# Kernel tuning notes

Measured on AMD Instinct MI355X. Metric: run time of the kernel, lower is better.

The kernel has to match this reference:

```python
import jax, jax.numpy as jnp
import numpy as np

DIM = 768
HEADS = 12
HIDDEN = int(DIM * 4.0)


def layernorm(x, w, b, eps=1e-5):
    mu = jnp.mean(x, axis=-1, keepdims=True)
    var = jnp.var(x, axis=-1, keepdims=True)
    return (x - mu) * jax.lax.rsqrt(var + eps) * w + b


def setup_inputs() -> dict:
    key = jax.random.key(0)
    ks = jax.random.split(key, 16)
    B, Nq, Nc, D = 4, 1024, 1024, DIM
    s = 0.02
    return {
        "query_tokens": jax.random.normal(ks[0], (B, Nq, D), jnp.float32),
        "context_tokens": jax.random.normal(ks[1], (B, Nc, D), jnp.float32),
        "wind_bias": jax.random.normal(ks[2], (B, 1, Nq, Nc), jnp.float32),
        "ln_q_w": jnp.ones((D,), jnp.float32), "ln_q_b": jnp.zeros((D,), jnp.float32),
        "ln_kv_w": jnp.ones((D,), jnp.float32), "ln_kv_b": jnp.zeros((D,), jnp.float32),
        "Wq": jax.random.normal(ks[3], (D, D), jnp.float32) * s, "bq": jnp.zeros((D,), jnp.float32),
        "Wk": jax.random.normal(ks[4], (D, D), jnp.float32) * s, "bk": jnp.zeros((D,), jnp.float32),
        "Wv": jax.random.normal(ks[5], (D, D), jnp.float32) * s, "bv": jnp.zeros((D,), jnp.float32),
        "Wo": jax.random.normal(ks[6], (D, D), jnp.float32) * s, "bo": jnp.zeros((D,), jnp.float32),
        "beta": jnp.ones((HEADS, 1, 1), jnp.float32),
        "ln_f_w": jnp.ones((D,), jnp.float32), "ln_f_b": jnp.zeros((D,), jnp.float32),
        "W1": jax.random.normal(ks[7], (D, HIDDEN), jnp.float32) * s, "b1": jnp.zeros((HIDDEN,), jnp.float32),
        "W2": jax.random.normal(ks[8], (HIDDEN, D), jnp.float32) * s, "b2": jnp.zeros((D,), jnp.float32),
    }


def reference(query_tokens, context_tokens, wind_bias,
              ln_q_w, ln_q_b, ln_kv_w, ln_kv_b,
              Wq, bq, Wk, bk, Wv, bv, Wo, bo, beta,
              ln_f_w, ln_f_b, W1, b1, W2, b2):
    B, Nq, D = query_tokens.shape
    H = HEADS
    hd = D // H
    scale = hd ** -0.5

    q = layernorm(query_tokens, ln_q_w, ln_q_b) @ Wq + bq
    kv = layernorm(context_tokens, ln_kv_w, ln_kv_b)
    k = kv @ Wk + bk
    v = kv @ Wv + bv

    # [B, H, N, hd]
    q = q.reshape(B, Nq, H, hd).transpose(0, 2, 1, 3)
    k = k.reshape(B, -1, H, hd).transpose(0, 2, 1, 3)
    v = v.reshape(B, -1, H, hd).transpose(0, 2, 1, 3)

    attn = jnp.einsum('bhqd,bhkd->bhqk', q * scale, k)
    attn = attn + beta * wind_bias  # beta: [H,1,1] broadcasts over [B,H,Nq,Nc]
    attn = jax.nn.softmax(attn.astype(jnp.float32), axis=-1).astype(q.dtype)

    out = jnp.einsum('bhqk,bhkd->bhqd', attn, v).transpose(0, 2, 1, 3).reshape(B, Nq, D)
    out = out @ Wo + bo

    x = query_tokens + out
    h = layernorm(x, ln_f_w, ln_f_b)
    h = jax.nn.gelu(h @ W1 + b1, approximate=False) @ W2 + b2
    return x + h
```

## Files before the change

### kernel.cpp

```cpp
#include <hip/hip_runtime.h>
#include <hip/hip_bf16.h>


#define DIM 768
#define HID 3072
#define NHEAD 12
#define BATCH 4
#define SEQ 1024
#define ROWS (BATCH * SEQ)
#define HD 64

typedef __attribute__((ext_vector_type(8))) __bf16 bf16x8;
typedef __attribute__((ext_vector_type(4))) float f32x4;
typedef __attribute__((ext_vector_type(4))) unsigned int u32x4;

#define MFMA16(a, b, c) __builtin_amdgcn_mfma_f32_16x16x32_bf16((a), (b), (c), 0, 0, 0)

#define GLDS16(g, l)                                                         \
  __builtin_amdgcn_global_load_lds(                                          \
      (const __attribute__((address_space(1))) void*)(g),                    \
      (__attribute__((address_space(3))) void*)(l), 16, 0, 0)

__device__ __forceinline__ unsigned pk2(float lo, float hi) {
  unsigned a = __bfloat16_as_ushort(__float2bfloat16(lo));
  unsigned b = __bfloat16_as_ushort(__float2bfloat16(hi));
  return a | (b << 16);
}

__global__ __launch_bounds__(256) void wg_transpose(const float* __restrict__ W,
                                                    __hip_bfloat16* __restrict__ WT,
                                                    int K, int N) {
  __shared__ float tile[32][33];
  const int tx = threadIdx.x & 31, ty = threadIdx.x >> 5;
  const int n0 = blockIdx.x * 32, k0 = blockIdx.y * 32;
#pragma unroll
  for (int i = 0; i < 4; i++)
    tile[ty + i * 8][tx] = W[(size_t)(k0 + ty + i * 8) * N + n0 + tx];
  __syncthreads();
#pragma unroll
  for (int i = 0; i < 4; i++)
    WT[(size_t)(n0 + ty + i * 8) * K + k0 + tx] = __float2bfloat16(tile[tx][ty + i * 8]);
}

__global__ void wg_bcat(const float* __restrict__ bq, const float* __restrict__ bk,
                        const float* __restrict__ bv, float* __restrict__ bc) {
  int i = blockIdx.x * 256 + threadIdx.x;
  if (i < 768) bc[i] = bq[i];
  else if (i < 1536) bc[i] = bk[i - 768];
  else if (i < 2304) bc[i] = bv[i - 1536];
}

__global__ __launch_bounds__(256) void wg_ln(const float* __restrict__ in,
                                             const float* __restrict__ w,
                                             const float* __restrict__ b,
                                             __hip_bfloat16* __restrict__ out) {
  int row = blockIdx.x;
  int t = threadIdx.x;
  const float* p = in + (size_t)row * DIM;
  float v0 = p[t], v1 = p[t + 256], v2 = p[t + 512];
  float s = v0 + v1 + v2;
  float q = v0 * v0 + v1 * v1 + v2 * v2;
#pragma unroll
  for (int d = 1; d < 64; d <<= 1) {
    s += __shfl_xor(s, d);
    q += __shfl_xor(q, d);
  }
  __shared__ float ss[4], sq[4];
  if ((t & 63) == 0) {
    ss[t >> 6] = s;
    sq[t >> 6] = q;
  }
  __syncthreads();
  s = ss[0] + ss[1] + ss[2] + ss[3];
  q = sq[0] + sq[1] + sq[2] + sq[3];
  float mu = s * (1.0f / DIM);
  float var = q * (1.0f / DIM) - mu * mu;
  float rs = rsqrtf(var + 1e-5f);
  __hip_bfloat16* o = out + (size_t)row * DIM;
  o[t] = __float2bfloat16((v0 - mu) * rs * w[t] + b[t]);
  o[t + 256] = __float2bfloat16((v1 - mu) * rs * w[t + 256] + b[t + 256]);
  o[t + 512] = __float2bfloat16((v2 - mu) * rs * w[t + 512] + b[t + 512]);
}

template <int MODE>
__global__ __launch_bounds__(512) void wg_gemm(const __hip_bfloat16* __restrict__ A,
                                               const __hip_bfloat16* __restrict__ BT,
                                               const float* __restrict__ bias,
                                               void* __restrict__ Cout,
                                               const float* __restrict__ resid,
                                               float* __restrict__ aux,
                                               int N, int Kloop, int Kstride, float p0) {
  __shared__ __hip_bfloat16 As[128 * 64];
  __shared__ __hip_bfloat16 Bs[128 * 64];
  const int t = threadIdx.x;
  const int lane = t & 63;
  const int wave = t >> 6;
  const int wr = wave >> 1, wc = wave & 1;
  const int lhi = lane >> 4, llo = lane & 15;
  const int nbn = N >> 7;
  const int bm = blockIdx.x / nbn, bn = blockIdx.x % nbn;
  const int koff = (MODE == 7) ? blockIdx.y * Kloop : 0;

  const __hip_bfloat16* Ause = A;
  if (MODE == 6 && bn >= 6) Ause = A + (size_t)ROWS * DIM;

  const int s0 = t, s1 = t + 512;
  const int sr0 = s0 >> 3, sg0 = ((s0 & 7) ^ (sr0 & 7)) * 8;
  const int sr1 = s1 >> 3, sg1 = ((s1 & 7) ^ (sr1 & 7)) * 8;
  const __hip_bfloat16* Ag = Ause + (size_t)(bm * 128) * Kstride + koff;
  const __hip_bfloat16* Bg = BT + (size_t)(bn * 128) * Kstride + koff;

  f32x4 zero = {0.f, 0.f, 0.f, 0.f};
  f32x4 acc[2][4];
#pragma unroll
  for (int i = 0; i < 2; i++)
#pragma unroll
    for (int j = 0; j < 4; j++) acc[i][j] = zero;

  for (int k0 = 0; k0 < Kloop; k0 += 64) {
    __syncthreads();
    GLDS16(Ag + (size_t)sr0 * Kstride + k0 + sg0, As + s0 * 8);
    GLDS16(Ag + (size_t)sr1 * Kstride + k0 + sg1, As + s1 * 8);
    GLDS16(Bg + (size_t)sr0 * Kstride + k0 + sg0, Bs + s0 * 8);
    GLDS16(Bg + (size_t)sr1 * Kstride + k0 + sg1, Bs + s1 * 8);
    __syncthreads();
    bf16x8 af[2][2], bfr[4][2];
#pragma unroll
    for (int i = 0; i < 2; i++) {
      const int row = wr * 32 + i * 16 + llo;
#pragma unroll
      for (int kk = 0; kk < 2; kk++)
        af[i][kk] = *reinterpret_cast<const bf16x8*>(
            &As[row * 64 + (((kk * 4 + lhi) ^ (row & 7)) << 3)]);
    }
#pragma unroll
    for (int j = 0; j < 4; j++) {
      const int row = wc * 64 + j * 16 + llo;
#pragma unroll
      for (int kk = 0; kk < 2; kk++)
        bfr[j][kk] = *reinterpret_cast<const bf16x8*>(
            &Bs[row * 64 + (((kk * 4 + lhi) ^ (row & 7)) << 3)]);
    }
    __builtin_amdgcn_s_setprio(1);
#pragma unroll
    for (int kk = 0; kk < 2; kk++)
#pragma unroll
      for (int i = 0; i < 2; i++)
#pragma unroll
        for (int j = 0; j < 4; j++)
          acc[i][j] = MFMA16(af[i][kk], bfr[j][kk], acc[i][j]);
    __builtin_amdgcn_s_setprio(0);
  }

#pragma unroll
  for (int i = 0; i < 2; i++) {
    int gr = bm * 128 + wr * 32 + i * 16 + lhi * 4;
#pragma unroll
    for (int j = 0; j < 4; j++) {
      int gc = bn * 128 + wc * 64 + j * 16 + llo;
      float bv_ = (MODE == 7) ? 0.f : bias[gc];
#pragma unroll
      for (int r = 0; r < 4; r++) {
        float v = acc[i][j][r] + bv_;
        int row = gr + r;
        size_t idx = (size_t)row * N + gc;
        if (MODE == 3) {
          aux[idx] = resid[idx] + v;
        } else if (MODE == 4) {
          ((__hip_bfloat16*)Cout)[idx] =
              __float2bfloat16(v * 0.5f * (1.0f + erff(v * 0.70710678118f)));
        } else if (MODE == 7) {
          aux[(size_t)blockIdx.y * ROWS * N + idx] = v;
        } else if (MODE == 6) {
          int sec = gc / 768;
          int n2 = gc - sec * 768;
          __hip_bfloat16* base = (__hip_bfloat16*)Cout;
          if (sec == 0) {
            base[(size_t)row * DIM + n2] = __float2bfloat16(v * p0);
          } else if (sec == 1) {
            base[(size_t)ROWS * DIM + (size_t)row * DIM + n2] = __float2bfloat16(v);
          } else {
            int b_ = row >> 10, n_ = row & 1023;
            int h_ = n2 >> 6, d_ = n2 & 63;
            base[(size_t)2 * ROWS * DIM +
                 (((size_t)(b_ * NHEAD + h_) * HD + d_) << 10) + n_] = __float2bfloat16(v);
          }
        }
      }
    }
  }
}

template <int NP>
__global__ __launch_bounds__(256) void wg_red(const float* __restrict__ partial,
                                              const float* __restrict__ resid,
                                              const float* __restrict__ bias,
                                              float* __restrict__ out) {
  const int i = blockIdx.x * 256 + threadIdx.x;
  const int NF4 = ROWS * DIM / 4;
  if (i >= NF4) return;
  const f32x4* P = (const f32x4*)partial;
  f32x4 p = P[i];
#pragma unroll
  for (int c = 1; c < NP; c++) p += P[i + c * NF4];
  f32x4 r = ((const f32x4*)resid)[i];
  f32x4 bv = ((const f32x4*)bias)[i % (DIM / 4)];
  ((f32x4*)out)[i] = r + p + bv;
}

__global__ __launch_bounds__(256) void wg_attn4(const __hip_bfloat16* __restrict__ Q,
                                                const __hip_bfloat16* __restrict__ Kb,
                                                const __hip_bfloat16* __restrict__ Vt,
                                                const float* __restrict__ wb,
                                                const float* __restrict__ beta,
                                                __hip_bfloat16* __restrict__ O) {
  __shared__ __hip_bfloat16 Ks[2][4096];
  __shared__ __hip_bfloat16 Vs[2][4096];
  const int t = threadIdx.x;
  const int lane = t & 63;
  const int lhi = lane >> 4, llo = lane & 15;

  const int bid = blockIdx.x;
  const int wid = (bid & 7) * 96 + (bid >> 3);
  const int h = wid % NHEAD;
  const int g = wid / NHEAD;
  const int qt = g & 15;
  const int b = g >> 4;
  const float betah = beta[h] * 1.44269504089f;

  const int w = t >> 6;
  const size_t qrow0 = (size_t)b * SEQ + qt * 64 + w * 16;
  const __hip_bfloat16* Qp = Q + qrow0 * DIM + h * HD;
  bf16x8 a0 = *reinterpret_cast<const bf16x8*>(&Qp[(size_t)llo * DIM + lhi * 8]);
  bf16x8 a1 = *reinterpret_cast<const bf16x8*>(&Qp[(size_t)llo * DIM + 32 + lhi * 8]);

  const __hip_bfloat16* Kg = Kb + (size_t)b * SEQ * DIM + h * HD;
  const __hip_bfloat16* Vg = Vt + (size_t)(b * NHEAD + h) * HD * SEQ;
  const float* wrow = wb + (qrow0 + llo) * SEQ;

  const int slot0 = t, slot1 = t + 256;
  const int r0 = slot0 >> 3, c0 = (slot0 & 7) ^ (r0 & 7);
  const int r1 = slot1 >> 3, c1 = (slot1 & 7) ^ (r1 & 7);

  auto stage = [&](int buf, int kb) {
    GLDS16(Kg + (size_t)(kb + r0) * DIM + c0 * 8, &Ks[buf][slot0 * 8]);
    GLDS16(Kg + (size_t)(kb + r1) * DIM + c1 * 8, &Ks[buf][slot1 * 8]);
    GLDS16(Vg + (size_t)r0 * SEQ + kb + c0 * 8, &Vs[buf][slot0 * 8]);
    GLDS16(Vg + (size_t)r1 * SEQ + kb + c1 * 8, &Vs[buf][slot1 * 8]);
  };

  f32x4 zero = {0.f, 0.f, 0.f, 0.f};
  f32x4 oc[4];
#pragma unroll
  for (int c = 0; c < 4; c++) oc[c] = zero;
  float m_ = -1e30f, l_ = 0.f;

  f32x4 wv[4];
#pragma unroll
  for (int c2 = 0; c2 < 4; c2++)
    wv[c2] = *reinterpret_cast<const f32x4*>(&wrow[c2 * 16 + lhi * 4]);

  stage(0, 0);
  __syncthreads();
  int cur = 0;

  const int srcA = (lane & 15) | ((lane & 16) << 1);
  const bool chi = (lane & 32) != 0;

  for (int kt = 0; kt < SEQ / 64; kt++) {
    const int kb = kt * 64;
    f32x4 wvn[4];
    if (kt < SEQ / 64 - 1) {
      stage(cur ^ 1, kb + 64);
#pragma unroll
      for (int c2 = 0; c2 < 4; c2++)
        wvn[c2] = *reinterpret_cast<const f32x4*>(&wrow[kb + 64 + c2 * 16 + lhi * 4]);
    }

    f32x4 sv[4];
    __builtin_amdgcn_s_setprio(1);
#pragma unroll
    for (int c2 = 0; c2 < 4; c2++) {
      const int row = c2 * 16 + llo;
      bf16x8 k0 = *reinterpret_cast<const bf16x8*>(
          &Ks[cur][((row << 3) + (lhi ^ (row & 7))) << 3]);
      bf16x8 k1 = *reinterpret_cast<const bf16x8*>(
          &Ks[cur][((row << 3) + ((4 + lhi) ^ (row & 7))) << 3]);
      f32x4 s_ = zero;
      s_ = MFMA16(k0, a0, s_);
      s_ = MFMA16(k1, a1, s_);
      sv[c2] = s_;
    }
    __builtin_amdgcn_s_setprio(0);

#pragma unroll
    for (int c2 = 0; c2 < 4; c2++)
#pragma unroll
      for (int r = 0; r < 4; r++) sv[c2][r] += betah * wv[c2][r];

    float mx;
    {
      f32x4 m4;
#pragma unroll
      for (int r = 0; r < 4; r++)
        m4[r] = fmaxf(fmaxf(sv[0][r], sv[1][r]), fmaxf(sv[2][r], sv[3][r]));
      mx = fmaxf(fmaxf(m4[0], m4[1]), fmaxf(m4[2], m4[3]));
      mx = fmaxf(mx, __shfl_xor(mx, 16));
      mx = fmaxf(mx, __shfl_xor(mx, 32));
    }

    const bool grow = __any(mx > m_);
    float corr = 1.f;
    if (grow) {
      float mn = fmaxf(m_, mx);
      corr = exp2f(m_ - mn);
      m_ = mn;
    }

#pragma unroll
    for (int c2 = 0; c2 < 4; c2++)
#pragma unroll
      for (int r = 0; r < 4; r++) sv[c2][r] = exp2f(sv[c2][r] - m_);
    f32x4 s4;
#pragma unroll
    for (int r = 0; r < 4; r++) s4[r] = (sv[0][r] + sv[1][r]) + (sv[2][r] + sv[3][r]);
    float rs = (s4[0] + s4[1]) + (s4[2] + s4[3]);
    rs += __shfl_xor(rs, 16);
    rs += __shfl_xor(rs, 32);
    l_ = l_ * corr + rs;

    if (grow) {
      float cr[4];
#pragma unroll
      for (int r = 0; r < 4; r++) cr[r] = __shfl(corr, lhi * 4 + r);
#pragma unroll
      for (int c = 0; c < 4; c++)
#pragma unroll
        for (int r = 0; r < 4; r++) oc[c][r] *= cr[r];
    }

    unsigned p01[4], p23[4];
#pragma unroll
    for (int c2 = 0; c2 < 4; c2++) {
      p01[c2] = pk2(sv[c2][0], sv[c2][1]);
      p23[c2] = pk2(sv[c2][2], sv[c2][3]);
    }
    unsigned a01_0A = (unsigned)__shfl((int)p01[0], srcA);
    unsigned a01_1A = (unsigned)__shfl((int)p01[1], srcA);
    unsigned a23_0A = (unsigned)__shfl((int)p23[0], srcA);
    unsigned a23_1A = (unsigned)__shfl((int)p23[1], srcA);
    unsigned a01_0B = (unsigned)__shfl((int)p01[0], srcA + 16);
    unsigned a01_1B = (unsigned)__shfl((int)p01[1], srcA + 16);
    unsigned a23_0B = (unsigned)__shfl((int)p23[0], srcA + 16);
    unsigned a23_1B = (unsigned)__shfl((int)p23[1], srcA + 16);
    unsigned b01_2A = (unsigned)__shfl((int)p01[2], srcA);
    unsigned b01_3A = (unsigned)__shfl((int)p01[3], srcA);
    unsigned b23_2A = (unsigned)__shfl((int)p23[2], srcA);
    unsigned b23_3A = (unsigned)__shfl((int)p23[3], srcA);
    unsigned b01_2B = (unsigned)__shfl((int)p01[2], srcA + 16);
    unsigned b01_3B = (unsigned)__shfl((int)p01[3], srcA + 16);
    unsigned b23_2B = (unsigned)__shfl((int)p23[2], srcA + 16);
    unsigned b23_3B = (unsigned)__shfl((int)p23[3], srcA + 16);
    u32x4 t0, t1;
    t0[0] = chi ? a01_1A : a01_0A;
    t0[1] = chi ? a23_1A : a23_0A;
    t0[2] = chi ? a01_1B : a01_0B;
    t0[3] = chi ? a23_1B : a23_0B;
    t1[0] = chi ? b01_3A : b01_2A;
    t1[1] = chi ? b23_3A : b23_2A;
    t1[2] = chi ? b01_3B : b01_2B;
    t1[3] = chi ? b23_3B : b23_2B;
    bf16x8 pf0 = __builtin_bit_cast(bf16x8, t0);
    bf16x8 pf1 = __builtin_bit_cast(bf16x8, t1);

    __builtin_amdgcn_s_setprio(1);
#pragma unroll
    for (int c = 0; c < 4; c++) {
      const int row = c * 16 + llo;
      bf16x8 v0 = *reinterpret_cast<const bf16x8*>(
          &Vs[cur][((row << 3) + (lhi ^ (row & 7))) << 3]);
      bf16x8 v1 = *reinterpret_cast<const bf16x8*>(
          &Vs[cur][((row << 3) + ((4 + lhi) ^ (row & 7))) << 3]);
      oc[c] = MFMA16(pf0, v0, oc[c]);
      oc[c] = MFMA16(pf1, v1, oc[c]);
    }
    __builtin_amdgcn_s_setprio(0);

    if (kt < SEQ / 64 - 1) {
#pragma unroll
      for (int c2 = 0; c2 < 4; c2++) wv[c2] = wvn[c2];
    }
    __syncthreads();
    cur ^= 1;
  }

  float iv[4];
  float invl = 1.0f / l_;
#pragma unroll
  for (int r = 0; r < 4; r++) iv[r] = __shfl(invl, lhi * 4 + r);
  __hip_bfloat16* Op = O + qrow0 * DIM + h * HD;
#pragma unroll
  for (int c = 0; c < 4; c++)
#pragma unroll
    for (int r = 0; r < 4; r++)
      Op[(size_t)(lhi * 4 + r) * DIM + c * 16 + llo] = __float2bfloat16(oc[c][r] * iv[r]);
}

extern "C" void kernel_launch(void* const* d_in, const int* in_sizes, int n_in,
                              void* d_out, int out_size, void* d_ws, size_t ws_size,
                              hipStream_t stream) {
  const float* query = (const float*)d_in[0];
  const float* context = (const float*)d_in[1];
  const float* wind = (const float*)d_in[2];
  const float* ln_q_w = (const float*)d_in[3];
  const float* ln_q_b = (const float*)d_in[4];
  const float* ln_kv_w = (const float*)d_in[5];
  const float* ln_kv_b = (const float*)d_in[6];
  const float* Wq = (const float*)d_in[7];
  const float* bq = (const float*)d_in[8];
  const float* Wk = (const float*)d_in[9];
  const float* bk = (const float*)d_in[10];
  const float* Wv = (const float*)d_in[11];
  const float* bv = (const float*)d_in[12];
  const float* Wo = (const float*)d_in[13];
  const float* bo = (const float*)d_in[14];
  const float* beta = (const float*)d_in[15];
  const float* ln_f_w = (const float*)d_in[16];
  const float* ln_f_b = (const float*)d_in[17];
  const float* W1 = (const float*)d_in[18];
  const float* b1 = (const float*)d_in[19];
  const float* W2 = (const float*)d_in[20];
  const float* b2 = (const float*)d_in[21];
  float* out = (float*)d_out;

  char* ws = (char*)d_ws;
  size_t off = 0;
  auto take = [&](size_t bytes) -> char* {
    char* p = ws + off;
    off += (bytes + 255) & ~(size_t)255;
    return p;
  };
  const size_t actB = (size_t)ROWS * DIM * 2;
  __hip_bfloat16* qln = (__hip_bfloat16*)take(actB);
  __hip_bfloat16* kvln = (__hip_bfloat16*)take(actB);
  __hip_bfloat16* qb = (__hip_bfloat16*)take(actB);
  __hip_bfloat16* kbuf = (__hip_bfloat16*)take(actB);
  __hip_bfloat16* vt = (__hip_bfloat16*)take(actB);
  __hip_bfloat16* aout = (__hip_bfloat16*)take(actB);
  __hip_bfloat16* hbuf = (__hip_bfloat16*)take(actB);
  float* xbuf = (float*)take((size_t)ROWS * DIM * 4);
  __hip_bfloat16* hid = (__hip_bfloat16*)take((size_t)ROWS * HID * 2);
  __hip_bfloat16* WqT = (__hip_bfloat16*)take((size_t)DIM * DIM * 2);
  __hip_bfloat16* WkT = (__hip_bfloat16*)take((size_t)DIM * DIM * 2);
  __hip_bfloat16* WvT = (__hip_bfloat16*)take((size_t)DIM * DIM * 2);
  __hip_bfloat16* WoT = (__hip_bfloat16*)take((size_t)DIM * DIM * 2);
  __hip_bfloat16* W1T = (__hip_bfloat16*)take((size_t)DIM * HID * 2);
  __hip_bfloat16* W2T = (__hip_bfloat16*)take((size_t)HID * DIM * 2);
  float* bcat = (float*)take(2304 * 4);
  float* kpart = (float*)take((size_t)4 * ROWS * DIM * 4);

  wg_transpose<<<dim3(24, 24), 256, 0, stream>>>(Wq, WqT, DIM, DIM);
  wg_transpose<<<dim3(24, 24), 256, 0, stream>>>(Wk, WkT, DIM, DIM);
  wg_transpose<<<dim3(24, 24), 256, 0, stream>>>(Wv, WvT, DIM, DIM);
  wg_transpose<<<dim3(24, 24), 256, 0, stream>>>(Wo, WoT, DIM, DIM);
  wg_transpose<<<dim3(96, 24), 256, 0, stream>>>(W1, W1T, DIM, HID);
  wg_transpose<<<dim3(24, 96), 256, 0, stream>>>(W2, W2T, HID, DIM);
  wg_bcat<<<9, 256, 0, stream>>>(bq, bk, bv, bcat);

  wg_ln<<<ROWS, 256, 0, stream>>>(query, ln_q_w, ln_q_b, qln);
  wg_ln<<<ROWS, 256, 0, stream>>>(context, ln_kv_w, ln_kv_b, kvln);

  const float scale = 0.125f * 1.44269504089f;
  wg_gemm<6><<<32 * 18, 512, 0, stream>>>(qln, WqT, bcat, qb, nullptr, nullptr,
                                          2304, DIM, DIM, scale);

  wg_attn4<<<768, 256, 0, stream>>>(qb, kbuf, vt, wind, beta, aout);

  const int g768 = (ROWS / 128) * (DIM / 128);
  const int g3072 = (ROWS / 128) * (HID / 128);
  wg_gemm<3><<<g768, 512, 0, stream>>>(aout, WoT, bo, nullptr, query, xbuf, DIM, DIM, DIM, 0.f);
  wg_ln<<<ROWS, 256, 0, stream>>>(xbuf, ln_f_w, ln_f_b, hbuf);
  wg_gemm<4><<<g3072, 512, 0, stream>>>(hbuf, W1T, b1, hid, nullptr, nullptr, HID, DIM, DIM, 0.f);
  wg_gemm<7><<<dim3(g768, 4), 512, 0, stream>>>(hid, W2T, nullptr, nullptr, nullptr, kpart,
                                                DIM, HID / 4, HID, 0.f);
  wg_red<4><<<(ROWS * DIM / 4 + 255) / 256, 256, 0, stream>>>(kpart, xbuf, b2, out);
}
```

Before: 225.2 us.

## Split attention KV tiles across waves with merged softmax and approximate GELU

The attention kernel now assigns each block 32 query rows and splits every 64-key tile between two wave pairs, halving per-wave score work and doubling the grid to raise parallelism. Partial outputs and softmax statistics are merged through shared memory at the end, and the P·V MFMA operand order is swapped so rescaling uses a per-lane scalar. The FFN GELU epilogue replaces erff with a sigmoid-of-cubic approximation to cut transcendental cost. This adds K/V reload traffic per query and introduces a small numeric deviation from exact GELU.

```diff
diff --git a/kernel.cpp b/kernel.cpp
--- a/kernel.cpp
+++ b/kernel.cpp
@@ -13,6 +13,7 @@
 typedef __attribute__((ext_vector_type(8))) __bf16 bf16x8;
 typedef __attribute__((ext_vector_type(4))) float f32x4;
 typedef __attribute__((ext_vector_type(4))) unsigned int u32x4;
+typedef __attribute__((ext_vector_type(2))) unsigned int u32x2;
 
 #define MFMA16(a, b, c) __builtin_amdgcn_mfma_f32_16x16x32_bf16((a), (b), (c), 0, 0, 0)
 
@@ -167,8 +168,10 @@
         if (MODE == 3) {
           aux[idx] = resid[idx] + v;
         } else if (MODE == 4) {
-          ((__hip_bfloat16*)Cout)[idx] =
-              __float2bfloat16(v * 0.5f * (1.0f + erff(v * 0.70710678118f)));
+          float x3 = v * v * v;
+          float z = -2.302208f * v - 0.102943f * x3;
+          float g = v / (1.0f + exp2f(z));
+          ((__hip_bfloat16*)Cout)[idx] = __float2bfloat16(g);
         } else if (MODE == 7) {
           aux[(size_t)blockIdx.y * ROWS * N + idx] = v;
         } else if (MODE == 6) {
@@ -208,7 +211,7 @@
   ((f32x4*)out)[i] = r + p + bv;
 }
 
-__global__ __launch_bounds__(256) void wg_attn4(const __hip_bfloat16* __restrict__ Q,
+__global__ __launch_bounds__(256) void wg_attn5(const __hip_bfloat16* __restrict__ Q,
                                                 const __hip_bfloat16* __restrict__ Kb,
                                                 const __hip_bfloat16* __restrict__ Vt,
                                                 const float* __restrict__ wb,
@@ -219,17 +222,19 @@
   const int t = threadIdx.x;
   const int lane = t & 63;
   const int lhi = lane >> 4, llo = lane & 15;
+  const int w = t >> 6;
+  const int wq = w & 1;
+  const int wk = w >> 1;
 
   const int bid = blockIdx.x;
-  const int wid = (bid & 7) * 96 + (bid >> 3);
+  const int wid = (bid & 7) * 192 + (bid >> 3);
   const int h = wid % NHEAD;
   const int g = wid / NHEAD;
-  const int qt = g & 15;
-  const int b = g >> 4;
+  const int qt = g & 31;
+  const int b = g >> 5;
   const float betah = beta[h] * 1.44269504089f;
 
-  const int w = t >> 6;
-  const size_t qrow0 = (size_t)b * SEQ + qt * 64 + w * 16;
+  const size_t qrow0 = (size_t)b * SEQ + qt * 32 + wq * 16;
   const __hip_bfloat16* Qp = Q + qrow0 * DIM + h * HD;
   bf16x8 a0 = *reinterpret_cast<const bf16x8*>(&Qp[(size_t)llo * DIM + lhi * 8]);
   bf16x8 a1 = *reinterpret_cast<const bf16x8*>(&Qp[(size_t)llo * DIM + 32 + lhi * 8]);
@@ -255,10 +260,12 @@
   for (int c = 0; c < 4; c++) oc[c] = zero;
   float m_ = -1e30f, l_ = 0.f;
 
-  f32x4 wv[4];
-#pragma unroll
-  for (int c2 = 0; c2 < 4; c2++)
-    wv[c2] = *reinterpret_cast<const f32x4*>(&wrow[c2 * 16 + lhi * 4]);
+  const int kvo = wk * 32;
+
+  f32x4 wv[2];
+#pragma unroll
+  for (int c2 = 0; c2 < 2; c2++)
+    wv[c2] = *reinterpret_cast<const f32x4*>(&wrow[kvo + c2 * 16 + lhi * 4]);
 
   stage(0, 0);
   __syncthreads();
@@ -269,19 +276,19 @@
 
   for (int kt = 0; kt < SEQ / 64; kt++) {
     const int kb = kt * 64;
-    f32x4 wvn[4];
+    f32x4 wvn[2];
     if (kt < SEQ / 64 - 1) {
       stage(cur ^ 1, kb + 64);
 #pragma unroll
-      for (int c2 = 0; c2 < 4; c2++)
-        wvn[c2] = *reinterpret_cast<const f32x4*>(&wrow[kb + 64 + c2 * 16 + lhi * 4]);
-    }
-
-    f32x4 sv[4];
+      for (int c2 = 0; c2 < 2; c2++)
+        wvn[c2] = *reinterpret_cast<const f32x4*>(&wrow[kb + 64 + kvo + c2 * 16 + lhi * 4]);
+    }
+
+    f32x4 sv[2];
     __builtin_amdgcn_s_setprio(1);
 #pragma unroll
-    for (int c2 = 0; c2 < 4; c2++) {
-      const int row = c2 * 16 + llo;
+    for (int c2 = 0; c2 < 2; c2++) {
+      const int row = kvo + c2 * 16 + llo;
       bf16x8 k0 = *reinterpret_cast<const bf16x8*>(
           &Ks[cur][((row << 3) + (lhi ^ (row & 7))) << 3]);
       bf16x8 k1 = *reinterpret_cast<const bf16x8*>(
@@ -294,7 +301,7 @@
     __builtin_amdgcn_s_setprio(0);
 
 #pragma unroll
-    for (int c2 = 0; c2 < 4; c2++)
+    for (int c2 = 0; c2 < 2; c2++)
 #pragma unroll
       for (int r = 0; r < 4; r++) sv[c2][r] += betah * wv[c2][r];
 
@@ -302,8 +309,7 @@
     {
       f32x4 m4;
 #pragma unroll
-      for (int r = 0; r < 4; r++)
-        m4[r] = fmaxf(fmaxf(sv[0][r], sv[1][r]), fmaxf(sv[2][r], sv[3][r]));
+      for (int r = 0; r < 4; r++) m4[r] = fmaxf(sv[0][r], sv[1][r]);
       mx = fmaxf(fmaxf(m4[0], m4[1]), fmaxf(m4[2], m4[3]));
       mx = fmaxf(mx, __shfl_xor(mx, 16));
       mx = fmaxf(mx, __shfl_xor(mx, 32));
@@ -318,92 +324,97 @@
     }
 
 #pragma unroll
-    for (int c2 = 0; c2 < 4; c2++)
+    for (int c2 = 0; c2 < 2; c2++)
 #pragma unroll
       for (int r = 0; r < 4; r++) sv[c2][r] = exp2f(sv[c2][r] - m_);
     f32x4 s4;
 #pragma unroll
-    for (int r = 0; r < 4; r++) s4[r] = (sv[0][r] + sv[1][r]) + (sv[2][r] + sv[3][r]);
+    for (int r = 0; r < 4; r++) s4[r] = sv[0][r] + sv[1][r];
     float rs = (s4[0] + s4[1]) + (s4[2] + s4[3]);
     rs += __shfl_xor(rs, 16);
     rs += __shfl_xor(rs, 32);
     l_ = l_ * corr + rs;
 
     if (grow) {
-      float cr[4];
-#pragma unroll
-      for (int r = 0; r < 4; r++) cr[r] = __shfl(corr, lhi * 4 + r);
 #pragma unroll
       for (int c = 0; c < 4; c++)
 #pragma unroll
-        for (int r = 0; r < 4; r++) oc[c][r] *= cr[r];
-    }
-
-    unsigned p01[4], p23[4];
-#pragma unroll
-    for (int c2 = 0; c2 < 4; c2++) {
+        for (int r = 0; r < 4; r++) oc[c][r] *= corr;
+    }
+
+    unsigned p01[2], p23[2];
+#pragma unroll
+    for (int c2 = 0; c2 < 2; c2++) {
       p01[c2] = pk2(sv[c2][0], sv[c2][1]);
       p23[c2] = pk2(sv[c2][2], sv[c2][3]);
     }
-    unsigned a01_0A = (unsigned)__shfl((int)p01[0], srcA);
-    unsigned a01_1A = (unsigned)__shfl((int)p01[1], srcA);
-    unsigned a23_0A = (unsigned)__shfl((int)p23[0], srcA);
-    unsigned a23_1A = (unsigned)__shfl((int)p23[1], srcA);
-    unsigned a01_0B = (unsigned)__shfl((int)p01[0], srcA + 16);
-    unsigned a01_1B = (unsigned)__shfl((int)p01[1], srcA + 16);
-    unsigned a23_0B = (unsigned)__shfl((int)p23[0], srcA + 16);
-    unsigned a23_1B = (unsigned)__shfl((int)p23[1], srcA + 16);
-    unsigned b01_2A = (unsigned)__shfl((int)p01[2], srcA);
-    unsigned b01_3A = (unsigned)__shfl((int)p01[3], srcA);
-    unsigned b23_2A = (unsigned)__shfl((int)p23[2], srcA);
-    unsigned b23_3A = (unsigned)__shfl((int)p23[3], srcA);
-    unsigned b01_2B = (unsigned)__shfl((int)p01[2], srcA + 16);
-    unsigned b01_3B = (unsigned)__shfl((int)p01[3], srcA + 16);
-    unsigned b23_2B = (unsigned)__shfl((int)p23[2], srcA + 16);
-    unsigned b23_3B = (unsigned)__shfl((int)p23[3], srcA + 16);
-    u32x4 t0, t1;
-    t0[0] = chi ? a01_1A : a01_0A;
-    t0[1] = chi ? a23_1A : a23_0A;
-    t0[2] = chi ? a01_1B : a01_0B;
-    t0[3] = chi ? a23_1B : a23_0B;
-    t1[0] = chi ? b01_3A : b01_2A;
-    t1[1] = chi ? b23_3A : b23_2A;
-    t1[2] = chi ? b01_3B : b01_2B;
-    t1[3] = chi ? b23_3B : b23_2B;
-    bf16x8 pf0 = __builtin_bit_cast(bf16x8, t0);
-    bf16x8 pf1 = __builtin_bit_cast(bf16x8, t1);
+    unsigned P01_0A = (unsigned)__shfl((int)p01[0], srcA);
+    unsigned P01_1A = (unsigned)__shfl((int)p01[1], srcA);
+    unsigned P23_0A = (unsigned)__shfl((int)p23[0], srcA);
+    unsigned P23_1A = (unsigned)__shfl((int)p23[1], srcA);
+    unsigned P01_0B = (unsigned)__shfl((int)p01[0], srcA + 16);
+    unsigned P01_1B = (unsigned)__shfl((int)p01[1], srcA + 16);
+    unsigned P23_0B = (unsigned)__shfl((int)p23[0], srcA + 16);
+    unsigned P23_1B = (unsigned)__shfl((int)p23[1], srcA + 16);
+    u32x4 tb;
+    tb[0] = chi ? P01_1A : P01_0A;
+    tb[1] = chi ? P23_1A : P23_0A;
+    tb[2] = chi ? P01_1B : P01_0B;
+    tb[3] = chi ? P23_1B : P23_0B;
+    bf16x8 pB = __builtin_bit_cast(bf16x8, tb);
 
     __builtin_amdgcn_s_setprio(1);
 #pragma unroll
     for (int c = 0; c < 4; c++) {
       const int row = c * 16 + llo;
-      bf16x8 v0 = *reinterpret_cast<const bf16x8*>(
-          &Vs[cur][((row << 3) + (lhi ^ (row & 7))) << 3]);
-      bf16x8 v1 = *reinterpret_cast<const bf16x8*>(
-          &Vs[cur][((row << 3) + ((4 + lhi) ^ (row & 7))) << 3]);
-      oc[c] = MFMA16(pf0, v0, oc[c]);
-      oc[c] = MFMA16(pf1, v1, oc[c]);
+      const int ch = (wk * 4 + lhi) ^ (row & 7);
+      bf16x8 vf = *reinterpret_cast<const bf16x8*>(&Vs[cur][((row << 3) + ch) << 3]);
+      oc[c] = MFMA16(vf, pB, oc[c]);
     }
     __builtin_amdgcn_s_setprio(0);
 
     if (kt < SEQ / 64 - 1) {
-#pragma unroll
-      for (int c2 = 0; c2 < 4; c2++) wv[c2] = wvn[c2];
+      wv[0] = wvn[0];
+      wv[1] = wvn[1];
     }
     __syncthreads();
     cur ^= 1;
   }
 
-  float iv[4];
-  float invl = 1.0f / l_;
-#pragma unroll
-  for (int r = 0; r < 4; r++) iv[r] = __shfl(invl, lhi * 4 + r);
-  __hip_bfloat16* Op = O + qrow0 * DIM + h * HD;
-#pragma unroll
-  for (int c = 0; c < 4; c++)
-#pragma unroll
-    for (int r = 0; r < 4; r++)
-      Op[(size_t)(lhi * 4 + r) * DIM + c * 16 + llo] = __float2bfloat16(oc[c][r] * iv[r]);
+  float* Obuf = (float*)&Ks[0][0];
+  float* Sbuf = (float*)&Vs[0][0];
+  if (wk == 1) {
+    if (lhi == 0) {
+      Sbuf[wq * 32 + llo] = m_;
+      Sbuf[wq * 32 + 16 + llo] = l_;
+    }
+    float* ob = Obuf + wq * 16 * 68 + llo * 68;
+#pragma unroll
+    for (int c = 0; c < 4; c++)
+      *reinterpret_cast<f32x4*>(&ob[c * 16 + lhi * 4]) = oc[c];
+  }
+  __syncthreads();
+  if (wk == 0) {
+    float m1 = Sbuf[wq * 32 + llo];
+    float l1 = Sbuf[wq * 32 + 16 + llo];
+    float mf = fmaxf(m_, m1);
+    float w0 = exp2f(m_ - mf), w1 = exp2f(m1 - mf);
+    float inv = 1.0f / (l_ * w0 + l1 * w1);
+    const float* ob = Obuf + wq * 16 * 68 + llo * 68;
+    __hip_bfloat16* Op = O + (qrow0 + llo) * DIM + h * HD;
+#pragma unroll
+    for (int c = 0; c < 4; c++) {
+      f32x4 o1 = *reinterpret_cast<const f32x4*>(&ob[c * 16 + lhi * 4]);
+      float v0 = (oc[c][0] * w0 + o1[0] * w1) * inv;
+      float v1 = (oc[c][1] * w0 + o1[1] * w1) * inv;
+      float v2 = (oc[c][2] * w0 + o1[2] * w1) * inv;
+      float v3 = (oc[c][3] * w0 + o1[3] * w1) * inv;
+      u32x2 pk;
+      pk[0] = pk2(v0, v1);
+      pk[1] = pk2(v2, v3);
+      *reinterpret_cast<u32x2*>(&Op[c * 16 + lhi * 4]) = pk;
+    }
+  }
 }
 
 extern "C" void kernel_launch(void* const* d_in, const int* in_sizes, int n_in,
@@ -474,7 +485,7 @@
   wg_gemm<6><<<32 * 18, 512, 0, stream>>>(qln, WqT, bcat, qb, nullptr, nullptr,
                                           2304, DIM, DIM, scale);
 
-  wg_attn4<<<768, 256, 0, stream>>>(qb, kbuf, vt, wind, beta, aout);
+  wg_attn5<<<1536, 256, 0, stream>>>(qb, kbuf, vt, wind, beta, aout);
 
   const int g768 = (ROWS / 128) * (DIM / 128);
   const int g3072 = (ROWS / 128) * (HID / 128);
```

Result: slower. 232.9 us (+3.4%).
